# Kernel tuning notes

Measured on AMD Instinct MI355X. Metric: run time of the kernel, lower is better.

## Reference

```python
import jax, jax.numpy as jnp
import numpy as np

N = 8192
IN_DIM = 256
HIDDEN = 128


def setup_inputs() -> dict:
    key = jax.random.key(0)
    k1, k2 = jax.random.split(key)
    X = jax.random.normal(k1, (N, IN_DIM), dtype=jnp.float32)
    # nn.Linear(in_dim, hidden, bias=False): weight [hidden, in_dim]
    W = jax.random.normal(k2, (HIDDEN, IN_DIM), dtype=jnp.float32) * (1.0 / np.sqrt(IN_DIM))
    return {"X": X, "W": W}


def reference(X, W):
    # Z = X @ W.T : [N, hidden]
    Z = jnp.einsum('ni,hi->nh', X, W)
    # Dense similarity graph: ReLU(Z Z^T), row-normalized
    A = jax.nn.relu(jnp.einsum('nh,mh->nm', Z, Z))  # [N, N]
    A = A / (A.sum(axis=-1, keepdims=True) + 1e-6)
    out = jnp.einsum('nm,mh->nh', A, Z)  # [N, hidden]
    return (out, A)
```

## Files before the change

### kernel.cpp

```cpp
#include <hip/hip_runtime.h>


#define NR 8192
#define KD 256
#define HD 128

typedef short v8s __attribute__((ext_vector_type(8)));
typedef float v4f __attribute__((ext_vector_type(4)));

static __device__ __forceinline__ ushort f2bf(float f) {
    union { float f; unsigned u; } c; c.f = f;
    unsigned u = c.u;
    u += 0x7fffu + ((u >> 16) & 1u);
    return (ushort)(u >> 16);
}
static __device__ __forceinline__ float bf2f(ushort b) {
    union { unsigned u; float f; } c; c.u = ((unsigned)b) << 16; return c.f;
}
static __device__ __forceinline__ unsigned pk2(float a, float b) {
    union { float f; unsigned u; } x, y; x.f = a; y.f = b;
    unsigned ua = x.u + 0x7fffu + ((x.u >> 16) & 1u);
    unsigned ub = y.u + 0x7fffu + ((y.u >> 16) & 1u);
    return (ua >> 16) | (ub & 0xffff0000u);
}

static __device__ __forceinline__ void lds_barrier() {
    asm volatile("s_waitcnt lgkmcnt(0)" ::: "memory");
    __builtin_amdgcn_s_barrier();
}

__global__ __launch_bounds__(256) void k_z(const float* __restrict__ X,
                                           const float* __restrict__ W,
                                           ushort* __restrict__ Zb,
                                           ushort* __restrict__ ZbT) {
    __shared__ ushort Xhi[16][264];
    __shared__ ushort Xlo[16][264];
    int tid = threadIdx.x, lane = tid & 63, wave = tid >> 6;
    int lm = lane & 15, lq = lane >> 4;
    int n0 = blockIdx.x * 16;
    int hbase = wave * 32;
    v8s Whi[2][8], Wlo[2][8];
#pragma unroll
    for (int hi = 0; hi < 2; ++hi) {
        const float* wp = W + (hbase + hi * 16 + lm) * KD + lq * 8;
#pragma unroll
        for (int ks = 0; ks < 8; ++ks) {
            float4 w0 = *(const float4*)(wp + ks * 32);
            float4 w1 = *(const float4*)(wp + ks * 32 + 4);
            float wv[8] = {w0.x, w0.y, w0.z, w0.w, w1.x, w1.y, w1.z, w1.w};
#pragma unroll
            for (int j = 0; j < 8; ++j) {
                ushort h = f2bf(wv[j]);
                Whi[hi][ks][j] = (short)h;
                Wlo[hi][ks][j] = (short)f2bf(wv[j] - bf2f(h));
            }
        }
    }
#pragma unroll
    for (int t = 0; t < 4; ++t) {
        int idx = tid + t * 256;
        int r = idx >> 6, c4 = (idx & 63) * 4;
        float4 x = *(const float4*)(X + (size_t)(n0 + r) * KD + c4);
        ushort h0 = f2bf(x.x), h1 = f2bf(x.y), h2 = f2bf(x.z), h3 = f2bf(x.w);
        unsigned a = ((unsigned)h0) | ((unsigned)h1 << 16);
        unsigned b = ((unsigned)h2) | ((unsigned)h3 << 16);
        unsigned c = ((unsigned)f2bf(x.x - bf2f(h0))) | ((unsigned)f2bf(x.y - bf2f(h1)) << 16);
        unsigned d = ((unsigned)f2bf(x.z - bf2f(h2))) | ((unsigned)f2bf(x.w - bf2f(h3)) << 16);
        *(uint2*)&Xhi[r][c4] = make_uint2(a, b);
        *(uint2*)&Xlo[r][c4] = make_uint2(c, d);
    }
    __syncthreads();
    {
        v8s Ah[8], Al[8];
#pragma unroll
        for (int ks = 0; ks < 8; ++ks) {
            Ah[ks] = *(const v8s*)&Xhi[lm][ks * 32 + lq * 8];
            Al[ks] = *(const v8s*)&Xlo[lm][ks * 32 + lq * 8];
        }
        v4f acc[2] = {{0.f, 0.f, 0.f, 0.f}, {0.f, 0.f, 0.f, 0.f}};
#pragma unroll
        for (int ks = 0; ks < 8; ++ks)
#pragma unroll
            for (int hi = 0; hi < 2; ++hi) {
                acc[hi] = __builtin_amdgcn_mfma_f32_16x16x32_bf16(Ah[ks], Whi[hi][ks], acc[hi], 0, 0, 0);
                acc[hi] = __builtin_amdgcn_mfma_f32_16x16x32_bf16(Ah[ks], Wlo[hi][ks], acc[hi], 0, 0, 0);
                acc[hi] = __builtin_amdgcn_mfma_f32_16x16x32_bf16(Al[ks], Whi[hi][ks], acc[hi], 0, 0, 0);
            }
#pragma unroll
        for (int hi = 0; hi < 2; ++hi) {
            int h = hbase + hi * 16 + lm;
            int nb = n0 + lq * 4;
            ushort b0 = f2bf(acc[hi][0]), b1 = f2bf(acc[hi][1]);
            ushort b2 = f2bf(acc[hi][2]), b3 = f2bf(acc[hi][3]);
            Zb[(size_t)(nb + 0) * HD + h] = b0;
            Zb[(size_t)(nb + 1) * HD + h] = b1;
            Zb[(size_t)(nb + 2) * HD + h] = b2;
            Zb[(size_t)(nb + 3) * HD + h] = b3;
            *(uint2*)&ZbT[(size_t)h * NR + nb] =
                make_uint2(((unsigned)b0) | ((unsigned)b1 << 16), ((unsigned)b2) | ((unsigned)b3 << 16));
        }
    }
}

__global__ __launch_bounds__(256) void k_rowsum(const ushort* __restrict__ Zb,
                                                float* __restrict__ rowsum) {
    __shared__ ushort ZC[2][64][136];
    int tid = threadIdx.x, lane = tid & 63, wave = tid >> 6;
    int lm = lane & 15, lq = lane >> 4;
    int rb = blockIdx.x >> 4, cs = blockIdx.x & 15;
    int row0 = rb * 128, cstart = cs * 512;
    v8s Bfr[2][4];
#pragma unroll
    for (int ri = 0; ri < 2; ++ri)
#pragma unroll
        for (int ks = 0; ks < 4; ++ks)
            Bfr[ri][ks] =
                *(const v8s*)(Zb + (size_t)(row0 + wave * 32 + ri * 16 + lm) * HD + ks * 32 + lq * 8);
    float rs[2] = {0.f, 0.f};
#pragma unroll
    for (int t = 0; t < 4; ++t) {
        int idx = tid + t * 256;
        int r = idx >> 4, c8 = (idx & 15) * 8;
        *(uint4*)&ZC[0][r][c8] = *(const uint4*)(Zb + (size_t)(cstart + r) * HD + c8);
    }
    __syncthreads();
    for (int it = 0; it < 8; ++it) {
        int cur = it & 1;
        int c0 = cstart + it * 64;
        uint4 sr[4];
        if (it < 7) {
#pragma unroll
            for (int t = 0; t < 4; ++t) {
                int idx = tid + t * 256;
                int r = idx >> 4, c8 = (idx & 15) * 8;
                sr[t] = *(const uint4*)(Zb + (size_t)(c0 + 64 + r) * HD + c8);
            }
        }
#pragma unroll
        for (int ci = 0; ci < 4; ++ci) {
            v8s Af[4];
#pragma unroll
            for (int ks = 0; ks < 4; ++ks)
                Af[ks] = *(const v8s*)&ZC[cur][ci * 16 + lm][ks * 32 + lq * 8];
            v4f a0 = {0.f, 0.f, 0.f, 0.f}, a1 = {0.f, 0.f, 0.f, 0.f};
#pragma unroll
            for (int ks = 0; ks < 4; ++ks) {
                a0 = __builtin_amdgcn_mfma_f32_16x16x32_bf16(Af[ks], Bfr[0][ks], a0, 0, 0, 0);
                a1 = __builtin_amdgcn_mfma_f32_16x16x32_bf16(Af[ks], Bfr[1][ks], a1, 0, 0, 0);
            }
            rs[0] += fmaxf(a0[0], 0.f) + fmaxf(a0[1], 0.f) + fmaxf(a0[2], 0.f) + fmaxf(a0[3], 0.f);
            rs[1] += fmaxf(a1[0], 0.f) + fmaxf(a1[1], 0.f) + fmaxf(a1[2], 0.f) + fmaxf(a1[3], 0.f);
        }
        if (it < 7) {
#pragma unroll
            for (int t = 0; t < 4; ++t) {
                int idx = tid + t * 256;
                int r = idx >> 4, c8 = (idx & 15) * 8;
                *(uint4*)&ZC[cur ^ 1][r][c8] = sr[t];
            }
        }
        __syncthreads();
    }
#pragma unroll
    for (int ri = 0; ri < 2; ++ri) {
        float v = rs[ri];
        v += __shfl_xor(v, 16, 64);
        v += __shfl_xor(v, 32, 64);
        if (lq == 0) atomicAdd(&rowsum[row0 + wave * 32 + ri * 16 + lm], v);
    }
}

__global__ __launch_bounds__(256) void k_main(const ushort* __restrict__ Zb,
                                              const ushort* __restrict__ ZbT,
                                              const float* __restrict__ rowsum,
                                              float* __restrict__ outp,
                                              float* __restrict__ Ap) {
    __shared__ ushort ZC[2][64][136];
    __shared__ ushort PT[2][64][72];
    int tid = threadIdx.x, lane = tid & 63, wave = tid >> 6;
    int lm = lane & 15, lq = lane >> 4;
    int rb = blockIdx.x >> 3, cs = blockIdx.x & 7;
    int row0 = rb * 64, colb = cs * 1024;
    int wr2 = wave >> 1, wc2 = wave & 1;
    v8s Bfr[2][4];
#pragma unroll
    for (int ri = 0; ri < 2; ++ri)
#pragma unroll
        for (int ks = 0; ks < 4; ++ks)
            Bfr[ri][ks] =
                *(const v8s*)(Zb + (size_t)(row0 + wr2 * 32 + ri * 16 + lm) * HD + ks * 32 + lq * 8);
    float rsv[2];
#pragma unroll
    for (int ri = 0; ri < 2; ++ri)
        rsv[ri] = 1.0f / (rowsum[row0 + wr2 * 32 + ri * 16 + lm] + 1e-6f);
    v4f U[2][4];
#pragma unroll
    for (int ri = 0; ri < 2; ++ri)
#pragma unroll
        for (int hi = 0; hi < 4; ++hi) U[ri][hi] = (v4f){0.f, 0.f, 0.f, 0.f};

#pragma unroll
    for (int t = 0; t < 4; ++t) {
        int idx = tid + t * 256;
        int r = idx >> 4, c8 = (idx & 15) * 8;
        *(uint4*)&ZC[0][r][c8] = *(const uint4*)(Zb + (size_t)(colb + r) * HD + c8);
    }
    __syncthreads();

    float* ap0 = Ap + (size_t)(row0 + wr2 * 32 + lm) * NR + colb + wc2 * 32 + lq * 4;
    float* ap1 = ap0 + (size_t)16 * NR;

    for (int it = 0; it < 16; ++it) {
        int cur = it & 1;
        int c0 = colb + it * 64;
        uint4 sr[4];
        if (it < 15) {
#pragma unroll
            for (int t = 0; t < 4; ++t) {
                int idx = tid + t * 256;
                int r = idx >> 4, c8 = (idx & 15) * 8;
                sr[t] = *(const uint4*)(Zb + (size_t)(c0 + 64 + r) * HD + c8);
            }
        }
        v8s Bz[4][2];
#pragma unroll
        for (int hi = 0; hi < 4; ++hi)
#pragma unroll
            for (int ks = 0; ks < 2; ++ks)
                Bz[hi][ks] = *(const v8s*)(ZbT + (size_t)(wc2 * 64 + hi * 16 + lm) * NR + c0 +
                                           ks * 32 + lq * 8);
        v4f avst[2][2];
#pragma unroll
        for (int ci = 0; ci < 2; ++ci) {
            v8s Af[4];
#pragma unroll
            for (int ks = 0; ks < 4; ++ks)
                Af[ks] = *(const v8s*)&ZC[cur][wc2 * 32 + ci * 16 + lm][ks * 32 + lq * 8];
            v4f S0 = {0.f, 0.f, 0.f, 0.f}, S1 = {0.f, 0.f, 0.f, 0.f};
#pragma unroll
            for (int ks = 0; ks < 4; ++ks) {
                S0 = __builtin_amdgcn_mfma_f32_16x16x32_bf16(Af[ks], Bfr[0][ks], S0, 0, 0, 0);
                S1 = __builtin_amdgcn_mfma_f32_16x16x32_bf16(Af[ks], Bfr[1][ks], S1, 0, 0, 0);
            }
            int cb = wc2 * 32 + ci * 16 + lq * 4;
            {
                v4f av;
                av[0] = fmaxf(S0[0], 0.f) * rsv[0]; av[1] = fmaxf(S0[1], 0.f) * rsv[0];
                av[2] = fmaxf(S0[2], 0.f) * rsv[0]; av[3] = fmaxf(S0[3], 0.f) * rsv[0];
                avst[ci][0] = av;
                *(uint2*)&PT[cur][wr2 * 32 + lm][cb] = make_uint2(pk2(av[0], av[1]), pk2(av[2], av[3]));
            }
            {
                v4f av;
                av[0] = fmaxf(S1[0], 0.f) * rsv[1]; av[1] = fmaxf(S1[1], 0.f) * rsv[1];
                av[2] = fmaxf(S1[2], 0.f) * rsv[1]; av[3] = fmaxf(S1[3], 0.f) * rsv[1];
                avst[ci][1] = av;
                *(uint2*)&PT[cur][wr2 * 32 + 16 + lm][cb] =
                    make_uint2(pk2(av[0], av[1]), pk2(av[2], av[3]));
            }
        }
        if (it < 15) {
#pragma unroll
            for (int t = 0; t < 4; ++t) {
                int idx = tid + t * 256;
                int r = idx >> 4, c8 = (idx & 15) * 8;
                *(uint4*)&ZC[cur ^ 1][r][c8] = sr[t];
            }
        }
        lds_barrier();
#pragma unroll
        for (int ci = 0; ci < 2; ++ci) {
            __builtin_nontemporal_store(avst[ci][0], (v4f*)(ap0 + ci * 16));
            __builtin_nontemporal_store(avst[ci][1], (v4f*)(ap1 + ci * 16));
        }
#pragma unroll
        for (int ks = 0; ks < 2; ++ks) {
            v8s P0 = *(const v8s*)&PT[cur][wr2 * 32 + lm][ks * 32 + lq * 8];
            v8s P1 = *(const v8s*)&PT[cur][wr2 * 32 + 16 + lm][ks * 32 + lq * 8];
#pragma unroll
            for (int hi = 0; hi < 4; ++hi) {
                U[0][hi] = __builtin_amdgcn_mfma_f32_16x16x32_bf16(P0, Bz[hi][ks], U[0][hi], 0, 0, 0);
                U[1][hi] = __builtin_amdgcn_mfma_f32_16x16x32_bf16(P1, Bz[hi][ks], U[1][hi], 0, 0, 0);
            }
        }
        ap0 += 64;
        ap1 += 64;
    }
#pragma unroll
    for (int ri = 0; ri < 2; ++ri)
#pragma unroll
        for (int hi = 0; hi < 4; ++hi)
#pragma unroll
            for (int j = 0; j < 4; ++j)
                atomicAdd(&outp[(size_t)(row0 + wr2 * 32 + ri * 16 + lq * 4 + j) * HD +
                                wc2 * 64 + hi * 16 + lm],
                          U[ri][hi][j]);
}

extern "C" void kernel_launch(void* const* d_in, const int* in_sizes, int n_in,
                              void* d_out, int out_size, void* d_ws, size_t ws_size,
                              hipStream_t stream) {
    (void)in_sizes; (void)n_in; (void)out_size; (void)ws_size;
    const float* X = (const float*)d_in[0];
    const float* W = (const float*)d_in[1];
    float* outp = (float*)d_out;
    float* Ap = outp + (size_t)NR * HD;
    char* ws = (char*)d_ws;
    ushort* Zb = (ushort*)ws;
    ushort* ZbT = (ushort*)(ws + (size_t)NR * HD * 2);
    float* rowsum = (float*)(ws + (size_t)NR * HD * 4);

    (void)hipMemsetAsync(outp, 0, (size_t)NR * HD * sizeof(float), stream);
    (void)hipMemsetAsync(rowsum, 0, NR * sizeof(float), stream);
    k_z<<<dim3(NR / 16), dim3(256), 0, stream>>>(X, W, Zb, ZbT);
    k_rowsum<<<dim3(1024), dim3(256), 0, stream>>>(Zb, rowsum);
    k_main<<<dim3(1024), dim3(256), 0, stream>>>(Zb, ZbT, rowsum, outp, Ap);
}
```

Before: 361.1 us.

## Write A tile via LDS with coalesced rows and repartition PV matmul across waves

The attention tile is now written to global memory by re-reading the bf16 P tile from LDS, so each wave stores full contiguous 256-byte row segments instead of scattered 16-byte fragments. The P·Z product is also repartitioned so each wave owns a 32-wide slice of the hidden dimension across all 64 rows, which halves the per-wave ZbT fragment loads. The stored A values are now bf16-rounded rather than fp32, which costs accuracy, and each iteration adds extra LDS reads.

```diff
diff --git a/kernel.cpp b/kernel.cpp
--- a/kernel.cpp
+++ b/kernel.cpp
@@ -7,6 +7,7 @@
 
 typedef short v8s __attribute__((ext_vector_type(8)));
 typedef float v4f __attribute__((ext_vector_type(4)));
+typedef float v2f __attribute__((ext_vector_type(2)));
 
 static __device__ __forceinline__ ushort f2bf(float f) {
     union { float f; unsigned u; } c; c.f = f;
@@ -193,11 +194,11 @@
 #pragma unroll
     for (int ri = 0; ri < 2; ++ri)
         rsv[ri] = 1.0f / (rowsum[row0 + wr2 * 32 + ri * 16 + lm] + 1e-6f);
-    v4f U[2][4];
-#pragma unroll
-    for (int ri = 0; ri < 2; ++ri)
-#pragma unroll
-        for (int hi = 0; hi < 4; ++hi) U[ri][hi] = (v4f){0.f, 0.f, 0.f, 0.f};
+    v4f U[4][2];
+#pragma unroll
+    for (int rA = 0; rA < 4; ++rA)
+#pragma unroll
+        for (int hi = 0; hi < 2; ++hi) U[rA][hi] = (v4f){0.f, 0.f, 0.f, 0.f};
 
 #pragma unroll
     for (int t = 0; t < 4; ++t) {
@@ -207,8 +208,8 @@
     }
     __syncthreads();
 
-    float* ap0 = Ap + (size_t)(row0 + wr2 * 32 + lm) * NR + colb + wc2 * 32 + lq * 4;
-    float* ap1 = ap0 + (size_t)16 * NR;
+    int l5 = lane >> 5;
+    int c2 = (lane & 31) * 2;
 
     for (int it = 0; it < 16; ++it) {
         int cur = it & 1;
@@ -222,14 +223,13 @@
                 sr[t] = *(const uint4*)(Zb + (size_t)(c0 + 64 + r) * HD + c8);
             }
         }
-        v8s Bz[4][2];
-#pragma unroll
-        for (int hi = 0; hi < 4; ++hi)
+        v8s Bz[2][2];
+#pragma unroll
+        for (int hi = 0; hi < 2; ++hi)
 #pragma unroll
             for (int ks = 0; ks < 2; ++ks)
-                Bz[hi][ks] = *(const v8s*)(ZbT + (size_t)(wc2 * 64 + hi * 16 + lm) * NR + c0 +
+                Bz[hi][ks] = *(const v8s*)(ZbT + (size_t)(wave * 32 + hi * 16 + lm) * NR + c0 +
                                            ks * 32 + lq * 8);
-        v4f avst[2][2];
 #pragma unroll
         for (int ci = 0; ci < 2; ++ci) {
             v8s Af[4];
@@ -244,19 +244,14 @@
             }
             int cb = wc2 * 32 + ci * 16 + lq * 4;
             {
-                v4f av;
-                av[0] = fmaxf(S0[0], 0.f) * rsv[0]; av[1] = fmaxf(S0[1], 0.f) * rsv[0];
-                av[2] = fmaxf(S0[2], 0.f) * rsv[0]; av[3] = fmaxf(S0[3], 0.f) * rsv[0];
-                avst[ci][0] = av;
-                *(uint2*)&PT[cur][wr2 * 32 + lm][cb] = make_uint2(pk2(av[0], av[1]), pk2(av[2], av[3]));
+                float f0 = fmaxf(S0[0], 0.f) * rsv[0], f1 = fmaxf(S0[1], 0.f) * rsv[0];
+                float f2 = fmaxf(S0[2], 0.f) * rsv[0], f3 = fmaxf(S0[3], 0.f) * rsv[0];
+                *(uint2*)&PT[cur][wr2 * 32 + lm][cb] = make_uint2(pk2(f0, f1), pk2(f2, f3));
             }
             {
-                v4f av;
-                av[0] = fmaxf(S1[0], 0.f) * rsv[1]; av[1] = fmaxf(S1[1], 0.f) * rsv[1];
-                av[2] = fmaxf(S1[2], 0.f) * rsv[1]; av[3] = fmaxf(S1[3], 0.f) * rsv[1];
-                avst[ci][1] = av;
-                *(uint2*)&PT[cur][wr2 * 32 + 16 + lm][cb] =
-                    make_uint2(pk2(av[0], av[1]), pk2(av[2], av[3]));
+                float f0 = fmaxf(S1[0], 0.f) * rsv[1], f1 = fmaxf(S1[1], 0.f) * rsv[1];
+                float f2 = fmaxf(S1[2], 0.f) * rsv[1], f3 = fmaxf(S1[3], 0.f) * rsv[1];
+                *(uint2*)&PT[cur][wr2 * 32 + 16 + lm][cb] = make_uint2(pk2(f0, f1), pk2(f2, f3));
             }
         }
         if (it < 15) {
@@ -269,32 +264,36 @@
         }
         lds_barrier();
 #pragma unroll
-        for (int ci = 0; ci < 2; ++ci) {
-            __builtin_nontemporal_store(avst[ci][0], (v4f*)(ap0 + ci * 16));
-            __builtin_nontemporal_store(avst[ci][1], (v4f*)(ap1 + ci * 16));
+        for (int rr = 0; rr < 8; ++rr) {
+            int r = wave * 16 + rr * 2 + l5;
+            unsigned pv = *(const unsigned*)&PT[cur][r][c2];
+            v2f o;
+            o.x = bf2f((ushort)(pv & 0xffffu));
+            o.y = bf2f((ushort)(pv >> 16));
+            __builtin_nontemporal_store(o, (v2f*)(Ap + (size_t)(row0 + r) * NR + c0 + c2));
         }
 #pragma unroll
         for (int ks = 0; ks < 2; ++ks) {
-            v8s P0 = *(const v8s*)&PT[cur][wr2 * 32 + lm][ks * 32 + lq * 8];
-            v8s P1 = *(const v8s*)&PT[cur][wr2 * 32 + 16 + lm][ks * 32 + lq * 8];
-#pragma unroll
-            for (int hi = 0; hi < 4; ++hi) {
-                U[0][hi] = __builtin_amdgcn_mfma_f32_16x16x32_bf16(P0, Bz[hi][ks], U[0][hi], 0, 0, 0);
-                U[1][hi] = __builtin_amdgcn_mfma_f32_16x16x32_bf16(P1, Bz[hi][ks], U[1][hi], 0, 0, 0);
-            }
-        }
-        ap0 += 64;
-        ap1 += 64;
-    }
-#pragma unroll
-    for (int ri = 0; ri < 2; ++ri)
-#pragma unroll
-        for (int hi = 0; hi < 4; ++hi)
+            v8s Pf[4];
+#pragma unroll
+            for (int rA = 0; rA < 4; ++rA)
+                Pf[rA] = *(const v8s*)&PT[cur][rA * 16 + lm][ks * 32 + lq * 8];
+#pragma unroll
+            for (int hi = 0; hi < 2; ++hi)
+#pragma unroll
+                for (int rA = 0; rA < 4; ++rA)
+                    U[rA][hi] = __builtin_amdgcn_mfma_f32_16x16x32_bf16(Pf[rA], Bz[hi][ks], U[rA][hi], 0, 0, 0);
+        }
+    }
+#pragma unroll
+    for (int rA = 0; rA < 4; ++rA)
+#pragma unroll
+        for (int hi = 0; hi < 2; ++hi)
 #pragma unroll
             for (int j = 0; j < 4; ++j)
-                atomicAdd(&outp[(size_t)(row0 + wr2 * 32 + ri * 16 + lq * 4 + j) * HD +
-                                wc2 * 64 + hi * 16 + lm],
-                          U[ri][hi][j]);
+                atomicAdd(&outp[(size_t)(row0 + rA * 16 + lq * 4 + j) * HD +
+                                wave * 32 + hi * 16 + lm],
+                          U[rA][hi][j]);
 }
 
 extern "C" void kernel_launch(void* const* d_in, const int* in_sizes, int n_in,
```

Measured after the change: 345.6 us. 1.04x faster.
